# Performance work log

Hardware: AMD Instinct MI355X
Metric: run time of the kernel (lower is better)

Reference implementation:

```python
import jax, jax.numpy as jnp
import numpy as np
import math

SCALE = 64.0
MARGIN = 0.5
THRESH = math.cos(math.pi - MARGIN)          # cos(pi - m)
MM = math.sin(math.pi - MARGIN) * MARGIN     # sin(pi - m) * m
N, D, C = 512, 512, 100000


def setup_inputs() -> dict:
    key = jax.random.key(0)
    k1, k2, k3 = jax.random.split(key, 3)
    x = jax.random.normal(k1, (N, D), dtype=jnp.float32)
    label = jax.random.randint(k2, (N,), 0, C, dtype=jnp.int64)
    # reset_parameters: uniform(-stdv, stdv), stdv = 1/sqrt(in_features)
    stdv = 1.0 / math.sqrt(D)
    weight = jax.random.uniform(k3, (C, D), dtype=jnp.float32, minval=-stdv, maxval=stdv)
    return {"input": x, "label": label, "weight": weight}


def reference(input, label, weight):
    # row-wise L2 normalize features and class weights
    ex = input / jnp.linalg.norm(input, axis=1, keepdims=True)
    ew = weight / jnp.linalg.norm(weight, axis=1, keepdims=True)
    cos = jnp.einsum("nd,cd->nc", ex, ew)               # [N, C]
    rows = jnp.arange(cos.shape[0])
    cos_l = cos[rows, label]                              # cos at the label column
    cond = cos_l > THRESH                                 # easy-margin condition per row
    onehot = (jnp.arange(cos.shape[1])[None, :] == label[:, None])
    a = jnp.where(onehot & cond[:, None], MARGIN, 0.0).astype(cos.dtype)
    b = jnp.where(onehot & (~cond[:, None]), -MM, 0.0).astype(cos.dtype)
    # clamp slightly inside [-1,1] to guard acos against fp roundoff
    cos_c = jnp.clip(cos, -1.0 + 1e-7, 1.0 - 1e-7)
    logits = SCALE * (jnp.cos(jnp.arccos(cos_c) + a) + b)
    return logits
```

## Files before the change

kernel.cpp:

```cpp
#include <hip/hip_runtime.h>
#include <hip/hip_bf16.h>
#include <stdint.h>


#define NROWS 512
#define DDIM 512
#define NCLS 100000
#define NCLS_PAD 100096

typedef __attribute__((ext_vector_type(8))) short bf16x8;
typedef __attribute__((ext_vector_type(4))) float f32x4;

__device__ __forceinline__ unsigned short f2bf(float x) {
    union { float f; uint32_t u; } c; c.f = x;
    uint32_t u = c.u;
    uint32_t r = (u + 0x7FFFu + ((u >> 16) & 1u)) >> 16;
    return (unsigned short)r;
}

__device__ __forceinline__ void g2lds16(const void* g, void* l) {
    __builtin_amdgcn_global_load_lds(
        (const __attribute__((address_space(1))) void*)g,
        (__attribute__((address_space(3))) void*)l,
        16, 0, 0);
}

__global__ __launch_bounds__(256)
void rownorm_bf16(const float* __restrict__ in, unsigned short* __restrict__ out,
                  int validRows, int totalRows) {
    const int row  = blockIdx.x * 4 + (threadIdx.x >> 6);
    const int lane = threadIdx.x & 63;
    if (row >= totalRows) return;

    unsigned short* orow = out + (size_t)row * DDIM;
    if (row >= validRows) {
        ushort4 z = {0, 0, 0, 0};
        *(ushort4*)(orow + lane * 4) = z;
        *(ushort4*)(orow + 256 + lane * 4) = z;
        return;
    }

    const float4* p = (const float4*)(in + (size_t)row * DDIM);
    float4 v0 = p[lane];
    float4 v1 = p[64 + lane];

    float ss = v0.x*v0.x + v0.y*v0.y + v0.z*v0.z + v0.w*v0.w
             + v1.x*v1.x + v1.y*v1.y + v1.z*v1.z + v1.w*v1.w;
    #pragma unroll
    for (int off = 32; off > 0; off >>= 1) ss += __shfl_xor(ss, off);
    const float r = rsqrtf(ss);

    ushort4 o0, o1;
    o0.x = f2bf(v0.x * r); o0.y = f2bf(v0.y * r);
    o0.z = f2bf(v0.z * r); o0.w = f2bf(v0.w * r);
    o1.x = f2bf(v1.x * r); o1.y = f2bf(v1.y * r);
    o1.z = f2bf(v1.z * r); o1.w = f2bf(v1.w * r);
    *(ushort4*)(orow + lane * 4) = o0;
    *(ushort4*)(orow + 256 + lane * 4) = o1;
}

__global__ __launch_bounds__(256)
void arcface_gemm(const unsigned short* __restrict__ A,
                  const unsigned short* __restrict__ B,
                  float* __restrict__ out) {
    __shared__ unsigned short As[128 * 32];
    __shared__ unsigned short Bs[128 * 32];

    const int t    = threadIdx.x;
    const int lane = t & 63;
    const int wid  = t >> 6;
    const int wr   = wid >> 1;
    const int wc   = wid & 1;
    const int rowBase = blockIdx.y * 128;
    const int colBase = blockIdx.x * 128;

    f32x4 acc[4][4] = {};

    const int r0 = t >> 2;
    const int c0 = (t & 3) << 3;
    const unsigned short* gA = A + (size_t)(rowBase + r0) * DDIM + c0;
    const unsigned short* gB = B + (size_t)(colBase + r0) * DDIM + c0;

    const int kg = (lane >> 4) << 3;
    const int fr = lane & 15;

    for (int kt = 0; kt < DDIM; kt += 32) {
        __syncthreads();
        g2lds16(gA + kt,                 &As[t * 8]);
        g2lds16(gA + kt + 64 * DDIM,     &As[2048 + t * 8]);
        g2lds16(gB + kt,                 &Bs[t * 8]);
        g2lds16(gB + kt + 64 * DDIM,     &Bs[2048 + t * 8]);
        __syncthreads();

        bf16x8 a[4], b[4];
        #pragma unroll
        for (int m = 0; m < 4; ++m)
            a[m] = *(const bf16x8*)&As[(wr * 64 + m * 16 + fr) * 32 + kg];
        #pragma unroll
        for (int n = 0; n < 4; ++n)
            b[n] = *(const bf16x8*)&Bs[(wc * 64 + n * 16 + fr) * 32 + kg];

        #pragma unroll
        for (int m = 0; m < 4; ++m)
            #pragma unroll
            for (int n = 0; n < 4; ++n)
                acc[m][n] = __builtin_amdgcn_mfma_f32_16x16x32_bf16(
                    a[m], b[n], acc[m][n], 0, 0, 0);
    }

    const float lo = -1.0f + 1e-7f, hi = 1.0f - 1e-7f;
    #pragma unroll
    for (int m = 0; m < 4; ++m) {
        const int r = rowBase + wr * 64 + m * 16 + (lane >> 4) * 4;
        #pragma unroll
        for (int n = 0; n < 4; ++n) {
            const int c = colBase + wc * 64 + n * 16 + fr;
            if (c < NCLS) {
                #pragma unroll
                for (int i = 0; i < 4; ++i) {
                    float v = acc[m][n][i];
                    v = fminf(fmaxf(v, lo), hi);
                    out[(size_t)(r + i) * NCLS + c] = 64.0f * v;
                }
            }
        }
    }
}

__global__ void arcface_fixup(const int* __restrict__ label, float* __restrict__ out) {
    const int n = blockIdx.x * 64 + threadIdx.x;
    if (n >= NROWS) return;
    const int c = label[n];
    const size_t idx = (size_t)n * NCLS + c;
    const float t = out[idx] * 0.015625f;
    const float COSM = 0.8775825618903728f;
    const float SINM = 0.479425538604203f;
    const float MM   = 0.2397127693021015f;
    const float THRESH = -0.8775825618903728f;
    float r;
    if (t > THRESH) {
        r = t * COSM - sqrtf(fmaxf(1.0f - t * t, 0.0f)) * SINM;
    } else {
        r = t - MM;
    }
    out[idx] = 64.0f * r;
}

extern "C" void kernel_launch(void* const* d_in, const int* in_sizes, int n_in,
                              void* d_out, int out_size, void* d_ws, size_t ws_size,
                              hipStream_t stream) {
    const float* x     = (const float*)d_in[0];
    const int*   label = (const int*)d_in[1];
    const float* w     = (const float*)d_in[2];
    float* out = (float*)d_out;

    unsigned short* Abf = (unsigned short*)d_ws;
    unsigned short* Wbf = (unsigned short*)d_ws + (size_t)NROWS * DDIM;

    rownorm_bf16<<<NROWS / 4, 256, 0, stream>>>(x, Abf, NROWS, NROWS);
    rownorm_bf16<<<NCLS_PAD / 4, 256, 0, stream>>>(w, Wbf, NCLS, NCLS_PAD);

    dim3 grid(NCLS_PAD / 128, NROWS / 128);
    arcface_gemm<<<grid, 256, 0, stream>>>(Abf, Wbf, out);

    arcface_fixup<<<(NROWS + 63) / 64, 64, 0, stream>>>(label, out);
}
```

Before: 431.8 us.

## Fuse weight normalization and bf16 conversion into the GEMM mainloop

Drops the separate weight row-normalize pass. The GEMM now loads fp32 weights directly, converts them to bf16 in registers, accumulates the squared norm while doing so, and applies the inverse norm in the epilogue. This avoids writing and rereading a bf16 copy of the weights. The grid is reordered so the four row-blocks that share one weight tile run next to each other, which helps L2 reuse. The B tile gets LDS padding, and the next chunk is prefetched into registers. In exchange, the weights are converted redundantly in each of the four row-blocks, and normalization now happens after the bf16 rounding rather than before it.

```diff
diff --git a/kernel.cpp b/kernel.cpp
--- a/kernel.cpp
+++ b/kernel.cpp
@@ -6,39 +6,27 @@
 #define NROWS 512
 #define DDIM 512
 #define NCLS 100000
-#define NCLS_PAD 100096
 
 typedef __attribute__((ext_vector_type(8))) short bf16x8;
+typedef __attribute__((ext_vector_type(8))) unsigned short u16x8;
 typedef __attribute__((ext_vector_type(4))) float f32x4;
 
 __device__ __forceinline__ unsigned short f2bf(float x) {
     union { float f; uint32_t u; } c; c.f = x;
-    uint32_t u = c.u;
-    uint32_t r = (u + 0x7FFFu + ((u >> 16) & 1u)) >> 16;
+    uint32_t r = (c.u + 0x7FFFu + ((c.u >> 16) & 1u)) >> 16;
     return (unsigned short)r;
 }
 
 __device__ __forceinline__ void g2lds16(const void* g, void* l) {
     __builtin_amdgcn_global_load_lds(
         (const __attribute__((address_space(1))) void*)g,
-        (__attribute__((address_space(3))) void*)l,
-        16, 0, 0);
+        (__attribute__((address_space(3))) void*)l, 16, 0, 0);
 }
 
 __global__ __launch_bounds__(256)
-void rownorm_bf16(const float* __restrict__ in, unsigned short* __restrict__ out,
-                  int validRows, int totalRows) {
+void rownorm_x(const float* __restrict__ in, unsigned short* __restrict__ out) {
     const int row  = blockIdx.x * 4 + (threadIdx.x >> 6);
     const int lane = threadIdx.x & 63;
-    if (row >= totalRows) return;
-
-    unsigned short* orow = out + (size_t)row * DDIM;
-    if (row >= validRows) {
-        ushort4 z = {0, 0, 0, 0};
-        *(ushort4*)(orow + lane * 4) = z;
-        *(ushort4*)(orow + 256 + lane * 4) = z;
-        return;
-    }
 
     const float4* p = (const float4*)(in + (size_t)row * DDIM);
     float4 v0 = p[lane];
@@ -50,6 +38,7 @@
     for (int off = 32; off > 0; off >>= 1) ss += __shfl_xor(ss, off);
     const float r = rsqrtf(ss);
 
+    unsigned short* orow = out + (size_t)row * DDIM;
     ushort4 o0, o1;
     o0.x = f2bf(v0.x * r); o0.y = f2bf(v0.y * r);
     o0.z = f2bf(v0.z * r); o0.w = f2bf(v0.w * r);
@@ -60,37 +49,72 @@
 }
 
 __global__ __launch_bounds__(256)
-void arcface_gemm(const unsigned short* __restrict__ A,
-                  const unsigned short* __restrict__ B,
-                  float* __restrict__ out) {
+void arcface_gemm_fused(const unsigned short* __restrict__ A,
+                        const float* __restrict__ W,
+                        float* __restrict__ out) {
     __shared__ unsigned short As[128 * 32];
-    __shared__ unsigned short Bs[128 * 32];
+    __shared__ unsigned short Bs[128 * 40];
+    __shared__ float sm[256];
 
     const int t    = threadIdx.x;
     const int lane = t & 63;
     const int wid  = t >> 6;
     const int wr   = wid >> 1;
     const int wc   = wid & 1;
-    const int rowBase = blockIdx.y * 128;
-    const int colBase = blockIdx.x * 128;
+    const int rowBase = blockIdx.x * 128;
+    const int colBase = blockIdx.y * 128;
 
     f32x4 acc[4][4] = {};
 
-    const int r0 = t >> 2;
-    const int c0 = (t & 3) << 3;
-    const unsigned short* gA = A + (size_t)(rowBase + r0) * DDIM + c0;
-    const unsigned short* gB = B + (size_t)(colBase + r0) * DDIM + c0;
+    const unsigned short* gA = A + (size_t)(rowBase + (t >> 2)) * DDIM + ((t & 3) << 3);
+
+    const int r0 = t >> 1;
+    const int cs = (t & 1) << 4;
+    const int bRow = colBase + r0;
+    const bool bValid = bRow < NCLS;
+    const float* gB = W + (size_t)bRow * DDIM + cs;
+    unsigned short* wB = &Bs[r0 * 40 + cs];
 
     const int kg = (lane >> 4) << 3;
     const int fr = lane & 15;
 
+    float ss = 0.0f;
+    float4 pf0, pf1, pf2, pf3;
+    if (bValid) {
+        pf0 = *(const float4*)(gB + 0);
+        pf1 = *(const float4*)(gB + 4);
+        pf2 = *(const float4*)(gB + 8);
+        pf3 = *(const float4*)(gB + 12);
+    } else {
+        pf0 = float4{0.f,0.f,0.f,0.f}; pf1 = pf0; pf2 = pf0; pf3 = pf0;
+    }
+
     for (int kt = 0; kt < DDIM; kt += 32) {
         __syncthreads();
-        g2lds16(gA + kt,                 &As[t * 8]);
-        g2lds16(gA + kt + 64 * DDIM,     &As[2048 + t * 8]);
-        g2lds16(gB + kt,                 &Bs[t * 8]);
-        g2lds16(gB + kt + 64 * DDIM,     &Bs[2048 + t * 8]);
+        g2lds16(gA + kt,             &As[t * 8]);
+        g2lds16(gA + kt + 64 * DDIM, &As[2048 + t * 8]);
+
+        ss += pf0.x*pf0.x + pf0.y*pf0.y + pf0.z*pf0.z + pf0.w*pf0.w;
+        ss += pf1.x*pf1.x + pf1.y*pf1.y + pf1.z*pf1.z + pf1.w*pf1.w;
+        ss += pf2.x*pf2.x + pf2.y*pf2.y + pf2.z*pf2.z + pf2.w*pf2.w;
+        ss += pf3.x*pf3.x + pf3.y*pf3.y + pf3.z*pf3.z + pf3.w*pf3.w;
+        u16x8 w0, w1;
+        w0[0] = f2bf(pf0.x); w0[1] = f2bf(pf0.y); w0[2] = f2bf(pf0.z); w0[3] = f2bf(pf0.w);
+        w0[4] = f2bf(pf1.x); w0[5] = f2bf(pf1.y); w0[6] = f2bf(pf1.z); w0[7] = f2bf(pf1.w);
+        w1[0] = f2bf(pf2.x); w1[1] = f2bf(pf2.y); w1[2] = f2bf(pf2.z); w1[3] = f2bf(pf2.w);
+        w1[4] = f2bf(pf3.x); w1[5] = f2bf(pf3.y); w1[6] = f2bf(pf3.z); w1[7] = f2bf(pf3.w);
+        *(u16x8*)(wB)     = w0;
+        *(u16x8*)(wB + 8) = w1;
+
         __syncthreads();
+
+        if (kt + 32 < DDIM && bValid) {
+            const float* g = gB + kt + 32;
+            pf0 = *(const float4*)(g + 0);
+            pf1 = *(const float4*)(g + 4);
+            pf2 = *(const float4*)(g + 8);
+            pf3 = *(const float4*)(g + 12);
+        }
 
         bf16x8 a[4], b[4];
         #pragma unroll
@@ -98,7 +122,7 @@
             a[m] = *(const bf16x8*)&As[(wr * 64 + m * 16 + fr) * 32 + kg];
         #pragma unroll
         for (int n = 0; n < 4; ++n)
-            b[n] = *(const bf16x8*)&Bs[(wc * 64 + n * 16 + fr) * 32 + kg];
+            b[n] = *(const bf16x8*)&Bs[(wc * 64 + n * 16 + fr) * 40 + kg];
 
         #pragma unroll
         for (int m = 0; m < 4; ++m)
@@ -108,7 +132,17 @@
                     a[m], b[n], acc[m][n], 0, 0, 0);
     }
 
+    sm[t] = ss;
+    __syncthreads();
+
     const float lo = -1.0f + 1e-7f, hi = 1.0f - 1e-7f;
+    float rn[4];
+    #pragma unroll
+    for (int n = 0; n < 4; ++n) {
+        const int cl = wc * 64 + n * 16 + fr;
+        rn[n] = rsqrtf(sm[cl * 2] + sm[cl * 2 + 1]);
+    }
+
     #pragma unroll
     for (int m = 0; m < 4; ++m) {
         const int r = rowBase + wr * 64 + m * 16 + (lane >> 4) * 4;
@@ -118,7 +152,7 @@
             if (c < NCLS) {
                 #pragma unroll
                 for (int i = 0; i < 4; ++i) {
-                    float v = acc[m][n][i];
+                    float v = acc[m][n][i] * rn[n];
                     v = fminf(fmaxf(v, lo), hi);
                     out[(size_t)(r + i) * NCLS + c] = 64.0f * v;
                 }
@@ -155,13 +189,11 @@
     float* out = (float*)d_out;
 
     unsigned short* Abf = (unsigned short*)d_ws;
-    unsigned short* Wbf = (unsigned short*)d_ws + (size_t)NROWS * DDIM;
 
-    rownorm_bf16<<<NROWS / 4, 256, 0, stream>>>(x, Abf, NROWS, NROWS);
-    rownorm_bf16<<<NCLS_PAD / 4, 256, 0, stream>>>(w, Wbf, NCLS, NCLS_PAD);
+    rownorm_x<<<NROWS / 4, 256, 0, stream>>>(x, Abf);
 
-    dim3 grid(NCLS_PAD / 128, NROWS / 128);
-    arcface_gemm<<<grid, 256, 0, stream>>>(Abf, Wbf, out);
+    dim3 grid(NROWS / 128, (NCLS + 127) / 128);
+    arcface_gemm_fused<<<grid, 256, 0, stream>>>(Abf, w, out);
 
     arcface_fixup<<<(NROWS + 63) / 64, 64, 0, stream>>>(label, out);
 }
```

New measurement: 423.8 us. About the same (-1.9%).

## Fuse weight normalization into GEMM with full-K LDS tile of W

Applied to the files above, without the earlier changes.

Removes the separate weight-normalization pass and its bf16 intermediate buffer. Each block of 512 threads now loads a 64-class strip of fp32 W, converts it to bf16 in padded LDS, and computes row norms to rescale the outputs after accumulation. The block covers all 512 rows, reading the small normalized A directly from global memory. This drops an extra read and write of W but makes the output scale depend on the unnormalized bf16 conversion, and the epilogue store pattern stays column-strided.

```diff
diff --git a/kernel.cpp b/kernel.cpp
--- a/kernel.cpp
+++ b/kernel.cpp
@@ -6,39 +6,23 @@
 #define NROWS 512
 #define DDIM 512
 #define NCLS 100000
-#define NCLS_PAD 100096
+#define BN 64
+#define BSTR 520
 
 typedef __attribute__((ext_vector_type(8))) short bf16x8;
+typedef __attribute__((ext_vector_type(8))) unsigned short u16x8;
 typedef __attribute__((ext_vector_type(4))) float f32x4;
 
 __device__ __forceinline__ unsigned short f2bf(float x) {
     union { float f; uint32_t u; } c; c.f = x;
-    uint32_t u = c.u;
-    uint32_t r = (u + 0x7FFFu + ((u >> 16) & 1u)) >> 16;
+    uint32_t r = (c.u + 0x7FFFu + ((c.u >> 16) & 1u)) >> 16;
     return (unsigned short)r;
 }
 
-__device__ __forceinline__ void g2lds16(const void* g, void* l) {
-    __builtin_amdgcn_global_load_lds(
-        (const __attribute__((address_space(1))) void*)g,
-        (__attribute__((address_space(3))) void*)l,
-        16, 0, 0);
-}
-
 __global__ __launch_bounds__(256)
-void rownorm_bf16(const float* __restrict__ in, unsigned short* __restrict__ out,
-                  int validRows, int totalRows) {
+void rownorm_x(const float* __restrict__ in, unsigned short* __restrict__ out) {
     const int row  = blockIdx.x * 4 + (threadIdx.x >> 6);
     const int lane = threadIdx.x & 63;
-    if (row >= totalRows) return;
-
-    unsigned short* orow = out + (size_t)row * DDIM;
-    if (row >= validRows) {
-        ushort4 z = {0, 0, 0, 0};
-        *(ushort4*)(orow + lane * 4) = z;
-        *(ushort4*)(orow + 256 + lane * 4) = z;
-        return;
-    }
 
     const float4* p = (const float4*)(in + (size_t)row * DDIM);
     float4 v0 = p[lane];
@@ -50,6 +34,7 @@
     for (int off = 32; off > 0; off >>= 1) ss += __shfl_xor(ss, off);
     const float r = rsqrtf(ss);
 
+    unsigned short* orow = out + (size_t)row * DDIM;
     ushort4 o0, o1;
     o0.x = f2bf(v0.x * r); o0.y = f2bf(v0.y * r);
     o0.z = f2bf(v0.z * r); o0.w = f2bf(v0.w * r);
@@ -59,47 +44,70 @@
     *(ushort4*)(orow + 256 + lane * 4) = o1;
 }
 
-__global__ __launch_bounds__(256)
-void arcface_gemm(const unsigned short* __restrict__ A,
-                  const unsigned short* __restrict__ B,
-                  float* __restrict__ out) {
-    __shared__ unsigned short As[128 * 32];
-    __shared__ unsigned short Bs[128 * 32];
+__global__ __launch_bounds__(512, 4)
+void arcface_gemm_fused(const unsigned short* __restrict__ A,
+                        const float* __restrict__ W,
+                        float* __restrict__ out) {
+    __shared__ unsigned short Bs[BN * BSTR];
+    __shared__ float ssp[BN * 8];
 
     const int t    = threadIdx.x;
     const int lane = t & 63;
     const int wid  = t >> 6;
-    const int wr   = wid >> 1;
-    const int wc   = wid & 1;
-    const int rowBase = blockIdx.y * 128;
-    const int colBase = blockIdx.x * 128;
+    const int fr   = lane & 15;
+    const int kg   = (lane >> 4) << 3;
+    const int colBase = blockIdx.x * BN;
+
+    const int prow  = (wid << 3) + (lane >> 3);
+    const int pcolB = (lane & 7) << 4;
+    const int cls   = colBase + prow;
+    const bool v    = cls < NCLS;
+    const float* gW = W + (size_t)cls * DDIM + pcolB;
+
+    float4 pf[16];
+    if (v) {
+        #pragma unroll
+        for (int c = 0; c < 4; ++c)
+            #pragma unroll
+            for (int j = 0; j < 4; ++j)
+                pf[c * 4 + j] = *(const float4*)(gW + c * 128 + j * 4);
+    } else {
+        #pragma unroll
+        for (int i = 0; i < 16; ++i) pf[i] = float4{0.f, 0.f, 0.f, 0.f};
+    }
+
+    float ss = 0.f;
+    #pragma unroll
+    for (int i = 0; i < 16; ++i)
+        ss += pf[i].x*pf[i].x + pf[i].y*pf[i].y + pf[i].z*pf[i].z + pf[i].w*pf[i].w;
+
+    #pragma unroll
+    for (int c = 0; c < 4; ++c) {
+        #pragma unroll
+        for (int h = 0; h < 2; ++h) {
+            const float4 p0 = pf[c * 4 + h * 2];
+            const float4 p1 = pf[c * 4 + h * 2 + 1];
+            u16x8 o;
+            o[0] = f2bf(p0.x); o[1] = f2bf(p0.y); o[2] = f2bf(p0.z); o[3] = f2bf(p0.w);
+            o[4] = f2bf(p1.x); o[5] = f2bf(p1.y); o[6] = f2bf(p1.z); o[7] = f2bf(p1.w);
+            *(u16x8*)&Bs[prow * BSTR + pcolB + c * 128 + h * 8] = o;
+        }
+    }
+    ssp[prow * 8 + (lane & 7)] = ss;
+    __syncthreads();
 
     f32x4 acc[4][4] = {};
+    const unsigned short* Ab = A + (size_t)(wid * 64 + fr) * DDIM + kg;
 
-    const int r0 = t >> 2;
-    const int c0 = (t & 3) << 3;
-    const unsigned short* gA = A + (size_t)(rowBase + r0) * DDIM + c0;
-    const unsigned short* gB = B + (size_t)(colBase + r0) * DDIM + c0;
-
-    const int kg = (lane >> 4) << 3;
-    const int fr = lane & 15;
-
+    #pragma unroll 4
     for (int kt = 0; kt < DDIM; kt += 32) {
-        __syncthreads();
-        g2lds16(gA + kt,                 &As[t * 8]);
-        g2lds16(gA + kt + 64 * DDIM,     &As[2048 + t * 8]);
-        g2lds16(gB + kt,                 &Bs[t * 8]);
-        g2lds16(gB + kt + 64 * DDIM,     &Bs[2048 + t * 8]);
-        __syncthreads();
-
         bf16x8 a[4], b[4];
         #pragma unroll
         for (int m = 0; m < 4; ++m)
-            a[m] = *(const bf16x8*)&As[(wr * 64 + m * 16 + fr) * 32 + kg];
+            a[m] = *(const bf16x8*)(Ab + (size_t)m * 16 * DDIM + kt);
         #pragma unroll
         for (int n = 0; n < 4; ++n)
-            b[n] = *(const bf16x8*)&Bs[(wc * 64 + n * 16 + fr) * 32 + kg];
-
+            b[n] = *(const bf16x8*)&Bs[(n * 16 + fr) * BSTR + kt + kg];
         #pragma unroll
         for (int m = 0; m < 4; ++m)
             #pragma unroll
@@ -109,18 +117,28 @@
     }
 
     const float lo = -1.0f + 1e-7f, hi = 1.0f - 1e-7f;
+    float rn[4];
+    #pragma unroll
+    for (int n = 0; n < 4; ++n) {
+        const int cl = n * 16 + fr;
+        float s = 0.f;
+        #pragma unroll
+        for (int j = 0; j < 8; ++j) s += ssp[cl * 8 + j];
+        rn[n] = rsqrtf(s);
+    }
+
     #pragma unroll
     for (int m = 0; m < 4; ++m) {
-        const int r = rowBase + wr * 64 + m * 16 + (lane >> 4) * 4;
+        const int r = wid * 64 + m * 16 + ((lane >> 4) << 2);
         #pragma unroll
         for (int n = 0; n < 4; ++n) {
-            const int c = colBase + wc * 64 + n * 16 + fr;
+            const int c = colBase + n * 16 + fr;
             if (c < NCLS) {
                 #pragma unroll
                 for (int i = 0; i < 4; ++i) {
-                    float v = acc[m][n][i];
-                    v = fminf(fmaxf(v, lo), hi);
-                    out[(size_t)(r + i) * NCLS + c] = 64.0f * v;
+                    float vv = acc[m][n][i] * rn[n];
+                    vv = fminf(fmaxf(vv, lo), hi);
+                    out[(size_t)(r + i) * NCLS + c] = 64.0f * vv;
                 }
             }
         }
@@ -155,13 +173,11 @@
     float* out = (float*)d_out;
 
     unsigned short* Abf = (unsigned short*)d_ws;
-    unsigned short* Wbf = (unsigned short*)d_ws + (size_t)NROWS * DDIM;
 
-    rownorm_bf16<<<NROWS / 4, 256, 0, stream>>>(x, Abf, NROWS, NROWS);
-    rownorm_bf16<<<NCLS_PAD / 4, 256, 0, stream>>>(w, Wbf, NCLS, NCLS_PAD);
+    rownorm_x<<<NROWS / 4, 256, 0, stream>>>(x, Abf);
 
-    dim3 grid(NCLS_PAD / 128, NROWS / 128);
-    arcface_gemm<<<grid, 256, 0, stream>>>(Abf, Wbf, out);
+    dim3 grid((NCLS + BN - 1) / BN);
+    arcface_gemm_fused<<<grid, 512, 0, stream>>>(Abf, w, out);
 
     arcface_fixup<<<(NROWS + 63) / 64, 64, 0, stream>>>(label, out);
 }
```

Measured after the change: 448.5 us. +3.9%, slower.
